# Optimization experiments

Measured on AMD Instinct MI355X. Metric: run time of the kernel, lower is better.

## Reference

```python
import jax, jax.numpy as jnp
import numpy as np
from jax import lax

BETA = 0.3

def setup_inputs() -> dict:
    key = jax.random.key(0)
    ks = jax.random.split(key, 5)
    B, C, H, W = 1, 64, 96, 96
    x = jax.random.normal(ks[0], (B, C, H, W), dtype=jnp.float32)
    # d_conv: Conv2d(C, C, k=3, stride=1, padding=2, dilation=2)
    dW = jax.random.normal(ks[1], (C, C, 3, 3), dtype=jnp.float32) * 0.05
    db = jax.random.normal(ks[2], (C,), dtype=jnp.float32) * 0.05
    # conv: Conv2d(C, C, k=1)
    cW = jax.random.normal(ks[3], (C, C, 1, 1), dtype=jnp.float32) * 0.1
    cb = jax.random.normal(ks[4], (C,), dtype=jnp.float32) * 0.05
    return {"x": x, "dW": dW, "db": db, "cW": cW, "cb": cb}

def _conv(x, w, b, padding, dilation):
    y = lax.conv_general_dilated(
        x, w, window_strides=(1, 1),
        padding=[(padding, padding), (padding, padding)],
        rhs_dilation=(dilation, dilation),
        dimension_numbers=("NCHW", "OIHW", "NCHW"))
    return y + b[None, :, None, None]

def reference(x, dW, db, cW, cb):
    B, C, H, W = x.shape
    HW = H * W
    y = _conv(x, dW, db, padding=2, dilation=2)   # (B,C,H,W), same d_conv used for q and k
    v = _conv(x, cW, cb, padding=0, dilation=1).reshape(B, HW, C)
    # NOTE: torch uses raw .reshape (not transpose) for q — faithful here.
    q = y.reshape(B, HW, C)
    k = y.reshape(B, C, HW)
    qk = jnp.einsum("bnc,bcm->bnm", q, k)         # (B,HW,HW)
    qk = jnp.where(jnp.abs(qk) > BETA, qk, 0.0)   # threshold mask (qk*mask)
    att = jax.nn.softmax(qk, axis=-1)
    att = jnp.einsum("bnm,bmc->bnc", att, v)      # (B,HW,C)
    att = att.swapaxes(1, 2).reshape(B, C, H, W)
    return x + att
```

## Files before the change

### kernel.cpp

```cpp
#include <hip/hip_runtime.h>
#include <hip/hip_bf16.h>

#define CC 64
#define HW 9216
#define IMG 96
#define SPLITS 16
#define SPLEN 576
#define ITERS 9
#define LOG2E 1.44269504f
#define RESC 5.545f

typedef _Float16 f16;
typedef __attribute__((ext_vector_type(8))) _Float16 f16x8;
typedef __attribute__((ext_vector_type(4))) _Float16 f16x4;
typedef __attribute__((ext_vector_type(4))) float f32x4;
typedef __attribute__((ext_vector_type(16))) float f32x16;
typedef __attribute__((ext_vector_type(4))) unsigned int u32x4;

#define GLOAD(gp, lp) __builtin_amdgcn_global_load_lds(                      \
    (const __attribute__((address_space(1))) void*)(gp),                     \
    (__attribute__((address_space(3))) void*)(lp), 16, 0, 0)

__global__ __launch_bounds__(256) void prepad_kernel(
    const float* __restrict__ x, const float* __restrict__ dW, const float* __restrict__ cW,
    f16* __restrict__ xt, f16* __restrict__ dWt, f16* __restrict__ cWt)
{
    __shared__ float tile[32][65];
    const int t = threadIdx.x;
    if (blockIdx.x >= 313) {
        const int wb = blockIdx.x - 313;
        #pragma unroll
        for (int j = 0; j < 4; ++j) {
            int idx = wb * 1024 + j * 256 + t;
            if (idx < 36864) {
                float val = dW[idx];
                int co = idx / 576;
                int r = idx - co * 576;
                int ci = r / 9, tap = r - ci * 9;
                dWt[tap * 4096 + co * 64 + ci] = (f16)val;
            } else {
                int c = idx - 36864;
                cWt[c] = (f16)cW[c];
            }
        }
        return;
    }
    const int p0 = blockIdx.x * 32;
    const int pl = t & 31;
    const int p = p0 + pl;
    int r = p / 100, c = p % 100;
    bool interior = (r >= 2) && (r < 98) && (c >= 2) && (c < 98);
    int img = (r - 2) * IMG + (c - 2);
    #pragma unroll
    for (int j = 0; j < 8; ++j) {
        int ci = j * 8 + (t >> 5);
        tile[pl][ci] = interior ? x[ci * HW + img] : 0.f;
    }
    __syncthreads();
    const int row16 = t >> 4, chunk = t & 15;
    #pragma unroll
    for (int j = 0; j < 2; ++j) {
        int row = j * 16 + row16;
        int pr = p0 + row;
        if (pr < 10000) {
            f16x4 hv = {(f16)tile[row][chunk * 4 + 0], (f16)tile[row][chunk * 4 + 1],
                        (f16)tile[row][chunk * 4 + 2], (f16)tile[row][chunk * 4 + 3]};
            *(f16x4*)&xt[pr * 64 + chunk * 4] = hv;
        }
    }
}

__global__ __launch_bounds__(64) void conv_mfma_kernel(
    const f16* __restrict__ xt, const f16* __restrict__ dWt, const float* __restrict__ db,
    const f16* __restrict__ cWt, const float* __restrict__ cb,
    f16* __restrict__ yq, f16* __restrict__ kt, f16* __restrict__ vt)
{
    const int b = blockIdx.x;
    const int tile = b >> 2, cog = b & 3;
    const int co0 = cog * 16;
    const int L = threadIdx.x;
    const int g = L >> 4, c16 = L & 15;

    f16x8 Bf[9][2], Bv[2];
    #pragma unroll
    for (int tap = 0; tap < 9; ++tap)
        #pragma unroll
        for (int kc = 0; kc < 2; ++kc)
            Bf[tap][kc] = *(const f16x8*)&dWt[(tap * 64 + co0 + c16) * 64 + g * 8 + kc * 32];
    #pragma unroll
    for (int kc = 0; kc < 2; ++kc)
        Bv[kc] = *(const f16x8*)&cWt[(co0 + c16) * 64 + g * 8 + kc * 32];

    const int ms = tile * 16;
    const int h = ms / IMG, wc = ms % IMG;
    const int pb = (h + 2) * 100 + (wc + 2) + c16;

    f32x4 accY = (f32x4){0.f, 0.f, 0.f, 0.f};
    f32x4 accV = (f32x4){0.f, 0.f, 0.f, 0.f};

    #pragma unroll
    for (int tap = 0; tap < 9; ++tap) {
        int kh = tap / 3, kw = tap % 3;
        int toff = (2 * kh - 2) * 100 + (2 * kw - 2);
        const f16* ap = xt + (pb + toff) * 64;
        f16x8 A0 = *(const f16x8*)(ap + g * 8);
        f16x8 A1 = *(const f16x8*)(ap + g * 8 + 32);
        accY = __builtin_amdgcn_mfma_f32_16x16x32_f16(A0, Bf[tap][0], accY, 0, 0, 0);
        accY = __builtin_amdgcn_mfma_f32_16x16x32_f16(A1, Bf[tap][1], accY, 0, 0, 0);
        if (tap == 4) {
            accV = __builtin_amdgcn_mfma_f32_16x16x32_f16(A0, Bv[0], accV, 0, 0, 0);
            accV = __builtin_amdgcn_mfma_f32_16x16x32_f16(A1, Bv[1], accV, 0, 0, 0);
        }
    }

    const float dbv = db[co0 + c16], cbv = cb[co0 + c16];
    f16 hy[4];
    #pragma unroll
    for (int j = 0; j < 4; ++j) hy[j] = (f16)(accY[j] + dbv);
    *(f16x4*)&yq[(co0 + c16) * HW + ms + 4 * g] = (f16x4){hy[0], hy[1], hy[2], hy[3]};
    #pragma unroll
    for (int j = 0; j < 4; ++j)
        kt[(ms + 4 * g + j) * 64 + co0 + c16] = hy[j];
    #pragma unroll
    for (int j = 0; j < 4; ++j) {
        int m = ms + 4 * g + j;
        vt[(m & 63) * HW + (co0 + c16) * 144 + (m >> 6)] = (f16)(accV[j] + cbv);
    }
}

__global__ __attribute__((amdgpu_waves_per_eu(4, 4))) __launch_bounds__(256)
void attn_kernel(
    const f16* __restrict__ kt, const f16* __restrict__ vt, const f16* __restrict__ yq,
    f16* __restrict__ acc_ws, float* __restrict__ m_ws, float* __restrict__ l_ws)
{
    __shared__ f16 sKT[2][64 * 64];
    __shared__ f16 sVT[2][64 * 64];
    __shared__ float sAL[4 * 32];

    const int t = threadIdx.x;
    const int L = t & 63, w = t >> 6;
    const int l5 = L >> 5, l31 = L & 31;
    const int x7 = l31 & 7;
    const int qb = blockIdx.x >> 4, sp = blockIdx.x & (SPLITS - 1);
    const int n0 = qb * 128;
    const int mbase = sp * SPLEN;
    float* alw = (float*)sAL + w * 32;

    const int g3 = L >> 3;
    const int gs = (L & 7) ^ g3;
    const int rb = w * 16;

    f16x8 qf[4];
    #pragma unroll
    for (int kc = 0; kc < 4; ++kc)
        qf[kc] = *(const f16x8*)(yq + (n0 + w * 32 + l31) * 64 + kc * 16 + l5 * 8);

    float mi = -1e30f, mtrue = -1e30f, li = 0.f;
    f32x16 acc[2];
    #pragma unroll
    for (int ct = 0; ct < 2; ++ct)
        #pragma unroll
        for (int r = 0; r < 16; ++r) acc[ct][r] = 0.f;

    GLOAD(kt + (mbase + rb + g3) * 64 + gs * 8,     &sKT[0][rb * 64]);
    GLOAD(kt + (mbase + rb + 8 + g3) * 64 + gs * 8, &sKT[0][(rb + 8) * 64]);
    GLOAD(vt + (rb + g3) * HW + mbase + gs * 8,     &sVT[0][rb * 64]);
    GLOAD(vt + (rb + 8 + g3) * HW + mbase + gs * 8, &sVT[0][(rb + 8) * 64]);

    for (int it = 0; it < ITERS; ++it) {
        const int cur = it & 1;
        __syncthreads();

        if (it + 1 < ITERS) {
            const int m1 = mbase + (it + 1) * 64;
            const int nx = cur ^ 1;
            GLOAD(kt + (m1 + rb + g3) * 64 + gs * 8,     &sKT[nx][rb * 64]);
            GLOAD(kt + (m1 + rb + 8 + g3) * 64 + gs * 8, &sKT[nx][(rb + 8) * 64]);
            GLOAD(vt + (rb + g3) * HW + m1 + gs * 8,     &sVT[nx][rb * 64]);
            GLOAD(vt + (rb + 8 + g3) * HW + m1 + gs * 8, &sVT[nx][(rb + 8) * 64]);
        }

        f32x16 st[2];
        #pragma unroll
        for (int kt2 = 0; kt2 < 2; ++kt2) {
            f32x16 d;
            #pragma unroll
            for (int r = 0; r < 16; ++r) d[r] = 0.f;
            #pragma unroll
            for (int kc = 0; kc < 4; ++kc) {
                f16x8 af = *(const f16x8*)&sKT[cur][(kt2 * 32 + l31) * 64 + ((((kc << 1) | l5) ^ x7) << 3)];
                d = __builtin_amdgcn_mfma_f32_32x32x16_f16(af, qf[kc], d, 0, 0, 0);
            }
            st[kt2] = d;
        }
        #pragma unroll
        for (int kt2 = 0; kt2 < 2; ++kt2)
            #pragma unroll
            for (int r = 0; r < 16; ++r)
                st[kt2][r] = (fabsf(st[kt2][r]) > 0.3f) ? st[kt2][r] : 0.f;

        float q8[8];
        #pragma unroll
        for (int kt2 = 0; kt2 < 2; ++kt2)
            #pragma unroll
            for (int rq = 0; rq < 4; ++rq)
                q8[kt2 * 4 + rq] = fmaxf(fmaxf(st[kt2][rq * 4 + 0], st[kt2][rq * 4 + 1]),
                                         fmaxf(st[kt2][rq * 4 + 2], st[kt2][rq * 4 + 3]));
        float mx = fmaxf(fmaxf(fmaxf(q8[0], q8[1]), fmaxf(q8[2], q8[3])),
                         fmaxf(fmaxf(q8[4], q8[5]), fmaxf(q8[6], q8[7])));
        mx = fmaxf(mx, __shfl_xor(mx, 32, 64));
        mtrue = fmaxf(mtrue, mx);

        unsigned long long need = __ballot(mx > mi + RESC);
        if (need) {
            float mnew = fmaxf(mi, mx);
            float alpha = __builtin_amdgcn_exp2f((mi - mnew) * LOG2E);
            li *= alpha;
            if (l5 == 0) alw[l31] = alpha;
            f32x4 aj[4];
            #pragma unroll
            for (int rq = 0; rq < 4; ++rq)
                aj[rq] = *(const f32x4*)&alw[rq * 8 + l5 * 4];
            #pragma unroll
            for (int ct = 0; ct < 2; ++ct)
                #pragma unroll
                for (int r = 0; r < 16; ++r)
                    acc[ct][r] *= aj[r >> 2][r & 3];
            mi = mnew;
        }
        const float nL = mi * LOG2E;

        float ls = 0.f;
        unsigned int u[2][4][2];
        #pragma unroll
        for (int kt2 = 0; kt2 < 2; ++kt2)
            #pragma unroll
            for (int rq = 0; rq < 4; ++rq) {
                float p0 = __builtin_amdgcn_exp2f(fmaf(st[kt2][rq * 4 + 0], LOG2E, -nL));
                float p1 = __builtin_amdgcn_exp2f(fmaf(st[kt2][rq * 4 + 1], LOG2E, -nL));
                float p2 = __builtin_amdgcn_exp2f(fmaf(st[kt2][rq * 4 + 2], LOG2E, -nL));
                float p3 = __builtin_amdgcn_exp2f(fmaf(st[kt2][rq * 4 + 3], LOG2E, -nL));
                ls += (p0 + p1) + (p2 + p3);
                u[kt2][rq][0] = __builtin_bit_cast(unsigned int, __builtin_amdgcn_cvt_pkrtz(p0, p1));
                u[kt2][rq][1] = __builtin_bit_cast(unsigned int, __builtin_amdgcn_cvt_pkrtz(p2, p3));
            }
        li += ls;

        #pragma unroll
        for (int kc = 0; kc < 4; ++kc) {
            const int kt2 = kc >> 1;
            const int rq0 = (kc & 1) * 2, rq1 = rq0 + 1;
            auto rA = __builtin_amdgcn_permlane32_swap(
                (int)u[kt2][rq0][0], (int)u[kt2][rq1][0], false, false);
            auto rB = __builtin_amdgcn_permlane32_swap(
                (int)u[kt2][rq0][1], (int)u[kt2][rq1][1], false, false);
            u32x4 pw = {(unsigned int)rA[0], (unsigned int)rB[0],
                        (unsigned int)rA[1], (unsigned int)rB[1]};
            f16x8 pa = __builtin_bit_cast(f16x8, pw);
            #pragma unroll
            for (int ct = 0; ct < 2; ++ct) {
                int vrow = ct * 32 + l31;
                f16x8 vb = *(const f16x8*)&sVT[cur][vrow * 64 + ((((kc << 1) | l5) ^ x7) << 3)];
                acc[ct] = __builtin_amdgcn_mfma_f32_32x32x16_f16(pa, vb, acc[ct], 0, 0, 0);
            }
        }
    }

    float fsc = __builtin_amdgcn_exp2f((mi - mtrue) * LOG2E);
    li *= fsc;
    float li_tot = li + __shfl_xor(li, 32, 64);
    if (l5 == 0) alw[l31] = fsc;
    f32x4 fj[4];
    #pragma unroll
    for (int rq = 0; rq < 4; ++rq)
        fj[rq] = *(const f32x4*)&alw[rq * 8 + l5 * 4];
    #pragma unroll
    for (int ct = 0; ct < 2; ++ct)
        #pragma unroll
        for (int r = 0; r < 16; ++r)
            acc[ct][r] *= fj[r >> 2][r & 3];

    const int base = blockIdx.x;
    #pragma unroll
    for (int ct = 0; ct < 2; ++ct)
        #pragma unroll
        for (int r = 0; r < 16; ++r) {
            int ql = w * 32 + (r & 3) + 8 * (r >> 2) + 4 * l5;
            int c  = ct * 32 + l31;
            acc_ws[base * 8192 + ql * 64 + c] = (f16)acc[ct][r];
        }
    if (l5 == 0) {
        m_ws[base * 128 + w * 32 + l31] = mtrue;
        l_ws[base * 128 + w * 32 + l31] = li_tot;
    }
}

__global__ __launch_bounds__(256) void merge_kernel(
    const f16* __restrict__ acc_ws, const float* __restrict__ m_ws, const float* __restrict__ l_ws,
    const float* __restrict__ x, float* __restrict__ out)
{
    __shared__ float wsh[SPLITS * 16];
    __shared__ float att[64 * 17];
    const int b = blockIdx.x;
    const int row0 = b * 16;
    const int qb = row0 >> 7;
    const int ql0 = row0 & 127;
    const int t = threadIdx.x;
    if (t < 16) {
        int ql = ql0 + t;
        float ms = -1e30f;
        float mv[SPLITS];
        #pragma unroll
        for (int sp = 0; sp < SPLITS; ++sp) {
            mv[sp] = m_ws[(qb * SPLITS + sp) * 128 + ql];
            ms = fmaxf(ms, mv[sp]);
        }
        float Lsum = 0.f, ev[SPLITS];
        #pragma unroll
        for (int sp = 0; sp < SPLITS; ++sp) {
            ev[sp] = __builtin_amdgcn_exp2f((mv[sp] - ms) * LOG2E);
            Lsum += l_ws[(qb * SPLITS + sp) * 128 + ql] * ev[sp];
        }
        float inv = 1.f / Lsum;
        #pragma unroll
        for (int sp = 0; sp < SPLITS; ++sp)
            wsh[sp * 16 + t] = ev[sp] * inv;
    }
    __syncthreads();
    {
        const int rr = t >> 4, c0 = (t & 15) * 4;
        float v0 = 0.f, v1 = 0.f, v2 = 0.f, v3 = 0.f;
        #pragma unroll
        for (int sp = 0; sp < SPLITS; ++sp) {
            f16x4 hv = *(const f16x4*)&acc_ws[(qb * SPLITS + sp) * 8192 + (ql0 + rr) * 64 + c0];
            float wv = wsh[sp * 16 + rr];
            v0 += (float)hv[0] * wv;
            v1 += (float)hv[1] * wv;
            v2 += (float)hv[2] * wv;
            v3 += (float)hv[3] * wv;
        }
        att[(c0 + 0) * 17 + rr] = v0;
        att[(c0 + 1) * 17 + rr] = v1;
        att[(c0 + 2) * 17 + rr] = v2;
        att[(c0 + 3) * 17 + rr] = v3;
    }
    __syncthreads();
    {
        const int c = t >> 2, r0 = (t & 3) * 4;
        const int idx = c * HW + row0 + r0;
        float4 xv = *(const float4*)&x[idx];
        float4 ov;
        ov.x = xv.x + att[c * 17 + r0 + 0];
        ov.y = xv.y + att[c * 17 + r0 + 1];
        ov.z = xv.z + att[c * 17 + r0 + 2];
        ov.w = xv.w + att[c * 17 + r0 + 3];
        *(float4*)&out[idx] = ov;
    }
}

extern "C" void kernel_launch(void* const* d_in, const int* in_sizes, int n_in,
                              void* d_out, int out_size, void* d_ws, size_t ws_size,
                              hipStream_t stream)
{
    const float* x  = (const float*)d_in[0];
    const float* dW = (const float*)d_in[1];
    const float* db = (const float*)d_in[2];
    const float* cW = (const float*)d_in[3];
    const float* cb = (const float*)d_in[4];
    float* out = (float*)d_out;

    char* ws = (char*)d_ws;
    f16* kt     = (f16*)(ws);
    f16* yq     = (f16*)(ws + 1179648);
    f16* vt     = (f16*)(ws + 2359296);
    f16* xt     = (f16*)(ws + 3538944);
    f16* dWt    = (f16*)(ws + 4818944);
    f16* cWt    = (f16*)(ws + 4892672);
    f16* acc_ws = (f16*)(ws + 4900864);
    float* m_ws = (float*)(ws + 23775232);
    float* l_ws = (float*)(ws + 24365056);

    prepad_kernel<<<dim3(353), dim3(256), 0, stream>>>(x, dW, cW, xt, dWt, cWt);
    conv_mfma_kernel<<<dim3(2304), dim3(64), 0, stream>>>(xt, dWt, db, cWt, cb, yq, kt, vt);
    attn_kernel<<<dim3(72 * SPLITS), dim3(256), 0, stream>>>(kt, vt, yq, acc_ws, m_ws, l_ws);
    merge_kernel<<<dim3(576), dim3(256), 0, stream>>>(acc_ws, m_ws, l_ws, x, out);
}
```

Measured before the change: 136.1 us.

## Replace double-buffered global_load_lds with single-buffer register-staged tile loads

The attention kernel's K/V tiles were double-buffered in LDS through direct global-to-LDS loads, which overlapped the next tile's fetch with compute. They now go through a single buffer filled by ordinary vector loads into registers, with an XOR-swizzled store and a second barrier each iteration. The online-softmax rescale is also moved after the exponentials so the alpha computation can overlap them, and the occupancy hint changes from waves_per_eu to launch_bounds. This halves LDS use and may let more blocks fit, but it gives up load/compute overlap and adds a sync per iteration.

```diff
diff --git a/kernel.cpp b/kernel.cpp
--- a/kernel.cpp
+++ b/kernel.cpp
@@ -16,10 +16,6 @@
 typedef __attribute__((ext_vector_type(4))) float f32x4;
 typedef __attribute__((ext_vector_type(16))) float f32x16;
 typedef __attribute__((ext_vector_type(4))) unsigned int u32x4;
-
-#define GLOAD(gp, lp) __builtin_amdgcn_global_load_lds(                      \
-    (const __attribute__((address_space(1))) void*)(gp),                     \
-    (__attribute__((address_space(3))) void*)(lp), 16, 0, 0)
 
 __global__ __launch_bounds__(256) void prepad_kernel(
     const float* __restrict__ x, const float* __restrict__ dW, const float* __restrict__ cW,
@@ -128,13 +124,12 @@
     }
 }
 
-__global__ __attribute__((amdgpu_waves_per_eu(4, 4))) __launch_bounds__(256)
-void attn_kernel(
+__global__ __launch_bounds__(256, 4) void attn_kernel(
     const f16* __restrict__ kt, const f16* __restrict__ vt, const f16* __restrict__ yq,
     f16* __restrict__ acc_ws, float* __restrict__ m_ws, float* __restrict__ l_ws)
 {
-    __shared__ f16 sKT[2][64 * 64];
-    __shared__ f16 sVT[2][64 * 64];
+    __shared__ f16 sKT[64 * 64];
+    __shared__ f16 sVT[64 * 64];
     __shared__ float sAL[4 * 32];
 
     const int t = threadIdx.x;
@@ -146,9 +141,10 @@
     const int mbase = sp * SPLEN;
     float* alw = (float*)sAL + w * 32;
 
-    const int g3 = L >> 3;
-    const int gs = (L & 7) ^ g3;
-    const int rb = w * 16;
+    const int srow0 = t >> 3, sch = t & 7;
+    const int srow1 = srow0 + 32;
+    const int dst0 = srow0 * 64 + ((sch ^ (srow0 & 7)) << 3);
+    const int dst1 = srow1 * 64 + ((sch ^ (srow1 & 7)) << 3);
 
     f16x8 qf[4];
     #pragma unroll
@@ -162,23 +158,14 @@
         #pragma unroll
         for (int r = 0; r < 16; ++r) acc[ct][r] = 0.f;
 
-    GLOAD(kt + (mbase + rb + g3) * 64 + gs * 8,     &sKT[0][rb * 64]);
-    GLOAD(kt + (mbase + rb + 8 + g3) * 64 + gs * 8, &sKT[0][(rb + 8) * 64]);
-    GLOAD(vt + (rb + g3) * HW + mbase + gs * 8,     &sVT[0][rb * 64]);
-    GLOAD(vt + (rb + 8 + g3) * HW + mbase + gs * 8, &sVT[0][(rb + 8) * 64]);
-
     for (int it = 0; it < ITERS; ++it) {
-        const int cur = it & 1;
+        const int m0 = mbase + it * 64;
         __syncthreads();
-
-        if (it + 1 < ITERS) {
-            const int m1 = mbase + (it + 1) * 64;
-            const int nx = cur ^ 1;
-            GLOAD(kt + (m1 + rb + g3) * 64 + gs * 8,     &sKT[nx][rb * 64]);
-            GLOAD(kt + (m1 + rb + 8 + g3) * 64 + gs * 8, &sKT[nx][(rb + 8) * 64]);
-            GLOAD(vt + (rb + g3) * HW + m1 + gs * 8,     &sVT[nx][rb * 64]);
-            GLOAD(vt + (rb + 8 + g3) * HW + m1 + gs * 8, &sVT[nx][(rb + 8) * 64]);
-        }
+        *(uint4*)&sKT[dst0] = *(const uint4*)&kt[(m0 + srow0) * 64 + sch * 8];
+        *(uint4*)&sKT[dst1] = *(const uint4*)&kt[(m0 + srow1) * 64 + sch * 8];
+        *(uint4*)&sVT[dst0] = *(const uint4*)&vt[srow0 * HW + m0 + sch * 8];
+        *(uint4*)&sVT[dst1] = *(const uint4*)&vt[srow1 * HW + m0 + sch * 8];
+        __syncthreads();
 
         f32x16 st[2];
         #pragma unroll
@@ -188,7 +175,7 @@
             for (int r = 0; r < 16; ++r) d[r] = 0.f;
             #pragma unroll
             for (int kc = 0; kc < 4; ++kc) {
-                f16x8 af = *(const f16x8*)&sKT[cur][(kt2 * 32 + l31) * 64 + ((((kc << 1) | l5) ^ x7) << 3)];
+                f16x8 af = *(const f16x8*)&sKT[(kt2 * 32 + l31) * 64 + ((((kc << 1) | l5) ^ x7) << 3)];
                 d = __builtin_amdgcn_mfma_f32_32x32x16_f16(af, qf[kc], d, 0, 0, 0);
             }
             st[kt2] = d;
@@ -212,23 +199,9 @@
         mtrue = fmaxf(mtrue, mx);
 
         unsigned long long need = __ballot(mx > mi + RESC);
-        if (need) {
-            float mnew = fmaxf(mi, mx);
-            float alpha = __builtin_amdgcn_exp2f((mi - mnew) * LOG2E);
-            li *= alpha;
-            if (l5 == 0) alw[l31] = alpha;
-            f32x4 aj[4];
-            #pragma unroll
-            for (int rq = 0; rq < 4; ++rq)
-                aj[rq] = *(const f32x4*)&alw[rq * 8 + l5 * 4];
-            #pragma unroll
-            for (int ct = 0; ct < 2; ++ct)
-                #pragma unroll
-                for (int r = 0; r < 16; ++r)
-                    acc[ct][r] *= aj[r >> 2][r & 3];
-            mi = mnew;
-        }
-        const float nL = mi * LOG2E;
+        float mnew = need ? fmaxf(mi, mx) : mi;
+        float nL = mnew * LOG2E;
+        float alpha = __builtin_amdgcn_exp2f(mi * LOG2E - nL);
 
         float ls = 0.f;
         unsigned int u[2][4][2];
@@ -244,7 +217,23 @@
                 u[kt2][rq][0] = __builtin_bit_cast(unsigned int, __builtin_amdgcn_cvt_pkrtz(p0, p1));
                 u[kt2][rq][1] = __builtin_bit_cast(unsigned int, __builtin_amdgcn_cvt_pkrtz(p2, p3));
             }
-        li += ls;
+
+        if (need) {
+            li = li * alpha + ls;
+            if (l5 == 0) alw[l31] = alpha;
+            f32x4 aj[4];
+            #pragma unroll
+            for (int rq = 0; rq < 4; ++rq)
+                aj[rq] = *(const f32x4*)&alw[rq * 8 + l5 * 4];
+            #pragma unroll
+            for (int ct = 0; ct < 2; ++ct)
+                #pragma unroll
+                for (int r = 0; r < 16; ++r)
+                    acc[ct][r] *= aj[r >> 2][r & 3];
+        } else {
+            li += ls;
+        }
+        mi = mnew;
 
         #pragma unroll
         for (int kc = 0; kc < 4; ++kc) {
@@ -260,7 +249,7 @@
             #pragma unroll
             for (int ct = 0; ct < 2; ++ct) {
                 int vrow = ct * 32 + l31;
-                f16x8 vb = *(const f16x8*)&sVT[cur][vrow * 64 + ((((kc << 1) | l5) ^ x7) << 3)];
+                f16x8 vb = *(const f16x8*)&sVT[vrow * 64 + ((((kc << 1) | l5) ^ x7) << 3)];
                 acc[ct] = __builtin_amdgcn_mfma_f32_32x32x16_f16(pa, vb, acc[ct], 0, 0, 0);
             }
         }
```

Measured after the change: 131.6 us. -3.3%, faster.
